# Kernel optimization log

Measured on AMD Instinct MI355X. Metric: run time of the kernel, lower is better.

Reference implementation:

```python
import jax, jax.numpy as jnp
import numpy as np

D_MODEL = 1024
N_HEADS = 16
D_K = D_MODEL // N_HEADS
D_FF = 4096
EPS = 1e-6


def setup_inputs() -> dict:
    key = jax.random.key(0)
    ks = jax.random.split(key, 8)
    s = 0.02
    return {
        "x": jax.random.normal(ks[0], (2, 2048, D_MODEL), dtype=jnp.float32),
        "Wq": jax.random.normal(ks[1], (D_MODEL, D_MODEL), dtype=jnp.float32) * s,
        "bq": jnp.zeros((D_MODEL,), jnp.float32),
        "Wk": jax.random.normal(ks[2], (D_MODEL, D_MODEL), dtype=jnp.float32) * s,
        "bk": jnp.zeros((D_MODEL,), jnp.float32),
        "Wv": jax.random.normal(ks[3], (D_MODEL, D_MODEL), dtype=jnp.float32) * s,
        "bv": jnp.zeros((D_MODEL,), jnp.float32),
        "Wo": jax.random.normal(ks[4], (D_MODEL, D_MODEL), dtype=jnp.float32) * s,
        "bo": jnp.zeros((D_MODEL,), jnp.float32),
        "W1": jax.random.normal(ks[5], (D_FF, D_MODEL), dtype=jnp.float32) * s,
        "b1": jnp.zeros((D_FF,), jnp.float32),
        "W2": jax.random.normal(ks[6], (D_MODEL, D_FF), dtype=jnp.float32) * s,
        "b2": jnp.zeros((D_MODEL,), jnp.float32),
        "g1": jnp.ones((D_MODEL,), jnp.float32),
        "be1": jnp.zeros((D_MODEL,), jnp.float32),
        "g2": jnp.ones((D_MODEL,), jnp.float32),
        "be2": jnp.zeros((D_MODEL,), jnp.float32),
    }


def _layernorm(x, gamma, beta):
    mean = x.mean(axis=-1, keepdims=True)
    var = ((x - mean) ** 2).mean(axis=-1, keepdims=True)
    return gamma * (x - mean) / jnp.sqrt(var + EPS) + beta


def _linear(x, W, b):
    # torch nn.Linear: y = x @ W.T + b
    return x @ W.T + b


def reference(x, Wq, bq, Wk, bk, Wv, bv, Wo, bo, W1, b1, W2, b2, g1, be1, g2, be2):
    B, S, _ = x.shape
    h = _layernorm(x, g1, be1)
    # project and split heads -> [B, H, S, d_k]
    Q = _linear(h, Wq, bq).reshape(B, S, N_HEADS, D_K).transpose(0, 2, 1, 3)
    K = _linear(h, Wk, bk).reshape(B, S, N_HEADS, D_K).transpose(0, 2, 1, 3)
    V = _linear(h, Wv, bv).reshape(B, S, N_HEADS, D_K).transpose(0, 2, 1, 3)
    scores = jnp.einsum("bhqd,bhkd->bhqk", Q, K) / jnp.sqrt(jnp.float32(D_K))
    attn = jax.nn.softmax(scores, axis=-1)
    ctx = jnp.einsum("bhqk,bhkd->bhqd", attn, V)
    ctx = ctx.transpose(0, 2, 1, 3).reshape(B, S, D_MODEL)
    x = x + _linear(ctx, Wo, bo)
    h2 = _layernorm(x, g2, be2)
    ff = _linear(jax.nn.gelu(_linear(h2, W1, b1), approximate=False), W2, b2)
    return x + ff
```

## Files before the change

kernel.cpp:

```cpp
#include <hip/hip_runtime.h>
#include <stdint.h>

#define D_MODEL 1024
#define N_HEADS 16
#define DKH     64
#define D_FF    4096
#define BATCH   2
#define SEQ     2048
#define M_TOK   (BATCH*SEQ)

typedef unsigned short u16;
typedef __attribute__((ext_vector_type(8))) short short8;
typedef __attribute__((ext_vector_type(4))) float f32x4;

__device__ __forceinline__ u16 f2b(float f){
  union { float f; uint32_t i; } c; c.f = f;
  uint32_t x = c.i;
  uint32_t r = x + 0x7fffu + ((x >> 16) & 1u);
  return (u16)(r >> 16);
}

__device__ __forceinline__ uint32_t pk_bf16(float a, float b){
  uint32_t d;
  asm("v_cvt_pk_bf16_f32 %0, %1, %2" : "=v"(d) : "v"(a), "v"(b));
  return d;
}

__device__ __forceinline__ void gl_lds16(const u16* g, u16* l){
  __builtin_amdgcn_global_load_lds(
      (const __attribute__((address_space(1))) void*)g,
      (__attribute__((address_space(3))) void*)l, 16, 0, 0);
}

#define MFMA16(a,b,c) __builtin_amdgcn_mfma_f32_16x16x32_bf16((a),(b),(c),0,0,0)

__global__ __launch_bounds__(256) void cvt_ln_kernel(
    const float* __restrict__ s0, const float* __restrict__ s1,
    const float* __restrict__ s2, const float* __restrict__ s3,
    const float* __restrict__ s4, const float* __restrict__ s5,
    u16* __restrict__ d0, u16* __restrict__ d1, u16* __restrict__ d2,
    u16* __restrict__ d3, u16* __restrict__ d4, u16* __restrict__ d5,
    const float* __restrict__ X, const float* __restrict__ G,
    const float* __restrict__ Bt, u16* __restrict__ O)
{
  __shared__ float psum[4], psum2[4];
  if (blockIdx.y == 6){
    const int row = blockIdx.x;
    const int t = threadIdx.x;
    float4 xv = *(const float4*)&X[(size_t)row * D_MODEL + t * 4];
    float s  = xv.x + xv.y + xv.z + xv.w;
    float s2 = xv.x*xv.x + xv.y*xv.y + xv.z*xv.z + xv.w*xv.w;
    #pragma unroll
    for (int off = 32; off >= 1; off >>= 1){
      s  += __shfl_down(s,  off, 64);
      s2 += __shfl_down(s2, off, 64);
    }
    const int wv = t >> 6, ln = t & 63;
    if (ln == 0){ psum[wv] = s; psum2[wv] = s2; }
    __syncthreads();
    float ts  = psum[0] + psum[1] + psum[2] + psum[3];
    float ts2 = psum2[0] + psum2[1] + psum2[2] + psum2[3];
    float mean = ts * (1.f / D_MODEL);
    float var  = ts2 * (1.f / D_MODEL) - mean * mean;
    float rstd = rsqrtf(var + 1e-6f);
    float4 g4 = *(const float4*)&G[t * 4];
    float4 b4 = *(const float4*)&Bt[t * 4];
    ushort4 o;
    o.x = f2b(g4.x * (xv.x - mean) * rstd + b4.x);
    o.y = f2b(g4.y * (xv.y - mean) * rstd + b4.y);
    o.z = f2b(g4.z * (xv.z - mean) * rstd + b4.z);
    o.w = f2b(g4.w * (xv.w - mean) * rstd + b4.w);
    *(ushort4*)&O[(size_t)row * D_MODEL + t * 4] = o;
    return;
  }
  const float* s; u16* d; int n;
  switch (blockIdx.y){
    case 0: s=s0; d=d0; n=D_MODEL*D_MODEL; break;
    case 1: s=s1; d=d1; n=D_MODEL*D_MODEL; break;
    case 2: s=s2; d=d2; n=D_MODEL*D_MODEL; break;
    case 3: s=s3; d=d3; n=D_MODEL*D_MODEL; break;
    case 4: s=s4; d=d4; n=D_FF*D_MODEL;   break;
    default: s=s5; d=d5; n=D_MODEL*D_FF;  break;
  }
  int i = (blockIdx.x * 256 + threadIdx.x) * 4;
  if (i < n){
    float4 f = *(const float4*)&s[i];
    ushort4 o; o.x = f2b(f.x); o.y = f2b(f.y); o.z = f2b(f.z); o.w = f2b(f.w);
    *(ushort4*)&d[i] = o;
  }
}

__global__ __launch_bounds__(256) void ln_kernel(
    const float* __restrict__ X, const float* __restrict__ G,
    const float* __restrict__ Bt, u16* __restrict__ O)
{
  const int row = blockIdx.x;
  const int t = threadIdx.x;
  float4 xv = *(const float4*)&X[(size_t)row * D_MODEL + t * 4];
  float s  = xv.x + xv.y + xv.z + xv.w;
  float s2 = xv.x*xv.x + xv.y*xv.y + xv.z*xv.z + xv.w*xv.w;
  #pragma unroll
  for (int off = 32; off >= 1; off >>= 1){
    s  += __shfl_down(s,  off, 64);
    s2 += __shfl_down(s2, off, 64);
  }
  __shared__ float psum[4], psum2[4];
  const int wv = t >> 6, ln = t & 63;
  if (ln == 0){ psum[wv] = s; psum2[wv] = s2; }
  __syncthreads();
  float ts  = psum[0] + psum[1] + psum[2] + psum[3];
  float ts2 = psum2[0] + psum2[1] + psum2[2] + psum2[3];
  float mean = ts * (1.f / D_MODEL);
  float var  = ts2 * (1.f / D_MODEL) - mean * mean;
  float rstd = rsqrtf(var + 1e-6f);
  float4 g4 = *(const float4*)&G[t * 4];
  float4 b4 = *(const float4*)&Bt[t * 4];
  ushort4 o;
  o.x = f2b(g4.x * (xv.x - mean) * rstd + b4.x);
  o.y = f2b(g4.y * (xv.y - mean) * rstd + b4.y);
  o.z = f2b(g4.z * (xv.z - mean) * rstd + b4.z);
  o.w = f2b(g4.w * (xv.w - mean) * rstd + b4.w);
  *(ushort4*)&O[(size_t)row * D_MODEL + t * 4] = o;
}

template<int EPI, int OUTF, int TM, int TN, int BK>
__global__ __launch_bounds__(256,2) void gemm_bt(
    const u16* __restrict__ A, const u16* __restrict__ W,
    const float* __restrict__ bias, const float* resid,
    void* Cout, int K, int Ndim)
{
  constexpr int MI = TM / 32;
  constexpr int NJ = TN / 32;
  constexpr int CPR = BK / 8;
  constexpr int RPI = 512 / BK;
  constexpr int nAw = TM * BK / 512 / 4;
  constexpr int nBw = TN * BK / 512 / 4;
  __shared__ __align__(16) u16 sA[TM*BK];
  __shared__ __align__(16) u16 sB[TN*BK];
  const int t = threadIdx.x;
  const int w = t >> 6, lane = t & 63, lr = lane & 15, quad = lane >> 4;
  const int wm = (w & 1) * (TM/2), wn = (w >> 1) * (TN/2);
  const int m0 = blockIdx.x * TM, n0 = blockIdx.y * TN;
  const int sub = lane / CPR;
  const int cl  = lane % CPR;

  f32x4 acc[MI][NJ];
  #pragma unroll
  for (int i = 0; i < MI; i++)
    #pragma unroll
    for (int j = 0; j < NJ; j++) acc[i][j] = (f32x4){0.f,0.f,0.f,0.f};

  for (int k0 = 0; k0 < K; k0 += BK){
    __syncthreads();
    #pragma unroll
    for (int it = 0; it < nAw; it++){
      int R = (w*nAw + it) * RPI;
      int gr = R + sub;
      int gc = (cl ^ (gr & 7)) * 8;
      gl_lds16(&A[(size_t)(m0 + gr) * K + k0 + gc], &sA[R * BK]);
    }
    #pragma unroll
    for (int it = 0; it < nBw; it++){
      int R = (w*nBw + it) * RPI;
      int gr = R + sub;
      int gc = (cl ^ (gr & 7)) * 8;
      gl_lds16(&W[(size_t)(n0 + gr) * K + k0 + gc], &sB[R * BK]);
    }
    __syncthreads();
    #pragma unroll
    for (int ks = 0; ks < BK/32; ks++){
      short8 af[MI], bfr[NJ];
      #pragma unroll
      for (int i = 0; i < MI; i++)
        af[i]  = *(const short8*)&sA[(wm + i*16 + lr)*BK + (((ks*4 + quad) ^ (lr & 7)) * 8)];
      #pragma unroll
      for (int j = 0; j < NJ; j++)
        bfr[j] = *(const short8*)&sB[(wn + j*16 + lr)*BK + (((ks*4 + quad) ^ (lr & 7)) * 8)];
      #pragma unroll
      for (int i = 0; i < MI; i++)
        #pragma unroll
        for (int j = 0; j < NJ; j++)
          acc[i][j] = MFMA16(af[i], bfr[j], acc[i][j]);
    }
  }

  #pragma unroll
  for (int j = 0; j < NJ; j++){
    int gn = n0 + wn + j*16 + lr;
    float bb = bias[gn];
    #pragma unroll
    for (int i = 0; i < MI; i++){
      #pragma unroll
      for (int r = 0; r < 4; r++){
        int gm = m0 + wm + i*16 + quad*4 + r;
        size_t idx = (size_t)gm * Ndim + gn;
        float v = acc[i][j][r] + bb;
        if (EPI == 1){
          float p = v * (1.59576912f + 0.07135481f * v * v);
          float e = __builtin_amdgcn_exp2f(-1.44269504f * p);
          v = v * __builtin_amdgcn_rcpf(1.f + e);
        }
        if (EPI == 2) v += resid[idx];
        if (OUTF) ((float*)Cout)[idx] = v;
        else      ((u16*)Cout)[idx] = f2b(v);
      }
    }
  }
}

__global__ __launch_bounds__(256,2) void gemm_qkv(
    const u16* __restrict__ A,
    const u16* __restrict__ Wq, const float* __restrict__ bq,
    const u16* __restrict__ Wk, const float* __restrict__ bk,
    const u16* __restrict__ Wv, const float* __restrict__ bv,
    u16* __restrict__ Qo, u16* __restrict__ Ko, u16* __restrict__ Vo)
{
  __shared__ __align__(16) u16 smem[2*128*64];
  u16* sA = smem;
  u16* sB = smem + 128*64;
  const u16* W; const float* bias; float scale;
  if (blockIdx.z == 0){ W = Wq; bias = bq; scale = 0.125f * 1.44269504f; }
  else if (blockIdx.z == 1){ W = Wk; bias = bk; scale = 1.f; }
  else { W = Wv; bias = bv; scale = 1.f; }

  const int t = threadIdx.x;
  const int w = t >> 6, lane = t & 63, lr = lane & 15, quad = lane >> 4;
  const int wm = (w & 1) * 64, wn = (w >> 1) * 64;
  const int m0 = blockIdx.x * 128, n0 = blockIdx.y * 128;
  const int srow = lane >> 3;
  const int scol = ((lane & 7) ^ srow) * 8;
  const int K = D_MODEL;

  f32x4 acc[4][4];
  #pragma unroll
  for (int i = 0; i < 4; i++)
    #pragma unroll
    for (int j = 0; j < 4; j++) acc[i][j] = (f32x4){0.f,0.f,0.f,0.f};

  for (int k0 = 0; k0 < K; k0 += 64){
    __syncthreads();
    #pragma unroll
    for (int it = 0; it < 4; it++){
      gl_lds16(&A[(size_t)(m0 + it*32 + w*8 + srow) * K + k0 + scol], &sA[(it*32 + w*8) * 64]);
      gl_lds16(&W[(size_t)(n0 + it*32 + w*8 + srow) * K + k0 + scol], &sB[(it*32 + w*8) * 64]);
    }
    __syncthreads();
    #pragma unroll
    for (int ks = 0; ks < 2; ks++){
      short8 af[4], bfr[4];
      #pragma unroll
      for (int i = 0; i < 4; i++)
        af[i]  = *(const short8*)&sA[(wm + i*16 + lr)*64 + (((ks*4 + quad) ^ (lr & 7)) * 8)];
      #pragma unroll
      for (int j = 0; j < 4; j++)
        bfr[j] = *(const short8*)&sB[(wn + j*16 + lr)*64 + (((ks*4 + quad) ^ (lr & 7)) * 8)];
      #pragma unroll
      for (int i = 0; i < 4; i++)
        #pragma unroll
        for (int j = 0; j < 4; j++)
          acc[i][j] = MFMA16(af[i], bfr[j], acc[i][j]);
    }
  }

  if (blockIdx.z == 2){
    __syncthreads();
    #pragma unroll
    for (int j = 0; j < 4; j++){
      int dl = wn + j*16 + lr;
      float bb = bias[n0 + dl];
      #pragma unroll
      for (int i = 0; i < 4; i++){
        #pragma unroll
        for (int r = 0; r < 4; r++){
          int tok = wm + i*16 + quad*4 + r;
          int phys = (((tok >> 3) ^ (dl & 7)) * 8) + (tok & 7);
          smem[dl*128 + phys] = f2b(acc[i][j][r] + bb);
        }
      }
    }
    __syncthreads();
    const int b = m0 >> 11, sq0 = m0 & 2047, hh0 = n0 >> 6;
    #pragma unroll
    for (int it = 0; it < 8; it++){
      int idx = it*256 + t;
      int drow = idx >> 4, c = idx & 15;
      float4 val = *(const float4*)&smem[drow*128 + ((c ^ (drow & 7)) * 8)];
      int hh = hh0 + (drow >> 6), d = drow & 63;
      *(float4*)&Vo[(((size_t)(b*N_HEADS + hh))*DKH + d)*SEQ + sq0 + c*8] = val;
    }
    return;
  }

  u16* out = (blockIdx.z == 0) ? Qo : Ko;
  #pragma unroll
  for (int j = 0; j < 4; j++){
    int gn = n0 + wn + j*16 + lr;
    int hh = gn >> 6, d = gn & 63;
    float bb = bias[gn];
    #pragma unroll
    for (int i = 0; i < 4; i++){
      #pragma unroll
      for (int r = 0; r < 4; r++){
        int gm = m0 + wm + i*16 + quad*4 + r;
        int b = gm >> 11, sq = gm & 2047;
        float v = (acc[i][j][r] + bb) * scale;
        out[(((size_t)(b * N_HEADS + hh)) * SEQ + sq) * DKH + d] = f2b(v);
      }
    }
  }
}

__global__ __launch_bounds__(512,2) void attn_kernel(
    const u16* __restrict__ Q, const u16* __restrict__ K,
    const u16* __restrict__ Vt, u16* __restrict__ ctx)
{
  __shared__ __align__(16) u16 sK[128*64];
  __shared__ __align__(16) u16 sVt[64*128];
  __shared__ __align__(16) u16 sP[8*16*128];

  const int t = threadIdx.x, w = t >> 6, lane = t & 63;
  const int lr = lane & 15, quad = lane >> 4;
  const int bh = blockIdx.x;
  const int q0 = blockIdx.y * 128;
  const u16* Qp = Q + ((size_t)bh * SEQ + q0) * DKH;
  const u16* Kp = K + (size_t)bh * SEQ * DKH;
  const u16* Vp = Vt + (size_t)bh * DKH * SEQ;

  short8 qf[2];
  #pragma unroll
  for (int ks = 0; ks < 2; ks++)
    qf[ks] = *(const short8*)&Qp[(size_t)(w*16 + lr) * DKH + ks*32 + quad*8];

  short8 ones;
  #pragma unroll
  for (int e = 0; e < 8; e++) ones[e] = (short)0x3F80;

  f32x4 acco[4];
  f32x4 accl;
  accl = (f32x4){0.f,0.f,0.f,0.f};
  #pragma unroll
  for (int jc = 0; jc < 4; jc++) acco[jc] = (f32x4){0.f,0.f,0.f,0.f};

  const int srow = lane >> 3;
  const int sc8  = ((lane & 7) ^ srow) * 8;
  const int lro  = lane >> 4, cl = lane & 15;

  for (int kt = 0; kt < SEQ/128; kt++){
    const int s0 = kt * 128;
    __syncthreads();
    #pragma unroll
    for (int it = 0; it < 2; it++)
      gl_lds16(&Kp[(size_t)(s0 + it*64 + w*8 + srow) * DKH + sc8],
               &sK[(it*64 + w*8) * 64]);
    #pragma unroll
    for (int it = 0; it < 2; it++){
      int R = w*8 + it*4;
      int gr = R + lro;
      int gc = (cl ^ (gr & 7)) * 8;
      gl_lds16(&Vp[(size_t)gr * SEQ + s0 + gc], &sVt[R * 128]);
    }
    __syncthreads();

    f32x4 st_[8];
    #pragma unroll
    for (int j = 0; j < 8; j++) st_[j] = (f32x4){0.f,0.f,0.f,0.f};
    #pragma unroll
    for (int ks = 0; ks < 2; ks++){
      #pragma unroll
      for (int j = 0; j < 8; j++){
        short8 kf = *(const short8*)&sK[(j*16 + lr)*64 + (((ks*4 + quad) ^ (lr & 7)) * 8)];
        st_[j] = MFMA16(kf, qf[ks], st_[j]);
      }
    }

    #pragma unroll
    for (int j = 0; j < 8; j++){
      float p0 = __builtin_amdgcn_exp2f(st_[j][0]);
      float p1 = __builtin_amdgcn_exp2f(st_[j][1]);
      float p2 = __builtin_amdgcn_exp2f(st_[j][2]);
      float p3 = __builtin_amdgcn_exp2f(st_[j][3]);
      uint2 pv; pv.x = pk_bf16(p0, p1); pv.y = pk_bf16(p2, p3);
      int c = j*2 + (quad >> 1);
      *(uint2*)&sP[w*2048 + lr*128 + ((c ^ (lr & 7)) * 8) + (quad & 1)*4] = pv;
    }

    #pragma unroll
    for (int ks = 0; ks < 4; ks++){
      short8 pf = *(const short8*)&sP[w*2048 + lr*128 + (((ks*4 + quad) ^ (lr & 7)) * 8)];
      accl = MFMA16(pf, ones, accl);
      #pragma unroll
      for (int jc = 0; jc < 4; jc++){
        short8 vf = *(const short8*)&sVt[(jc*16 + lr)*128 + (((ks*4 + quad) ^ (lr & 7)) * 8)];
        acco[jc] = MFMA16(pf, vf, acco[jc]);
      }
    }
  }

  const int bq = bh >> 4, hh = bh & 15;
  u16* op = ctx + ((size_t)bq * SEQ + q0) * D_MODEL + hh * DKH;
  #pragma unroll
  for (int r = 0; r < 4; r++){
    float rl = 1.f / accl[r];
    int row = w*16 + quad*4 + r;
    #pragma unroll
    for (int jc = 0; jc < 4; jc++)
      op[(size_t)row * D_MODEL + jc*16 + lr] = f2b(acco[jc][r] * rl);
  }
}

extern "C" void kernel_launch(void* const* d_in, const int* in_sizes, int n_in,
                              void* d_out, int out_size, void* d_ws, size_t ws_size,
                              hipStream_t stream)
{
  const float* x   = (const float*)d_in[0];
  const float* Wq  = (const float*)d_in[1];
  const float* bq  = (const float*)d_in[2];
  const float* Wk  = (const float*)d_in[3];
  const float* bk  = (const float*)d_in[4];
  const float* Wv  = (const float*)d_in[5];
  const float* bv  = (const float*)d_in[6];
  const float* Wo  = (const float*)d_in[7];
  const float* bo  = (const float*)d_in[8];
  const float* W1  = (const float*)d_in[9];
  const float* b1  = (const float*)d_in[10];
  const float* W2  = (const float*)d_in[11];
  const float* b2  = (const float*)d_in[12];
  const float* g1  = (const float*)d_in[13];
  const float* be1 = (const float*)d_in[14];
  const float* g2  = (const float*)d_in[15];
  const float* be2 = (const float*)d_in[16];

  char* ws = (char*)d_ws;
  const size_t MB = 1024ull * 1024ull;
  u16* wqb = (u16*)(ws + 0*MB);
  u16* wkb = (u16*)(ws + 2*MB);
  u16* wvb = (u16*)(ws + 4*MB);
  u16* wob = (u16*)(ws + 6*MB);
  u16* w1b = (u16*)(ws + 8*MB);
  u16* w2b = (u16*)(ws + 16*MB);
  u16* h   = (u16*)(ws + 24*MB);
  u16* q   = (u16*)(ws + 32*MB);
  u16* k   = (u16*)(ws + 40*MB);
  u16* ctx = (u16*)(ws + 48*MB);
  u16* vt  = (u16*)(ws + 56*MB);
  u16* ff  = (u16*)(ws + 32*MB);
  u16* h2  = h;
  float* x1 = (float*)d_out;

  cvt_ln_kernel<<<dim3(4096, 7), 256, 0, stream>>>(
      Wq, Wk, Wv, Wo, W1, W2, wqb, wkb, wvb, wob, w1b, w2b,
      x, g1, be1, h);

  gemm_qkv<<<dim3(M_TOK/128, D_MODEL/128, 3), 256, 0, stream>>>(
      h, wqb, bq, wkb, bk, wvb, bv, q, k, vt);
  attn_kernel<<<dim3(BATCH*N_HEADS, SEQ/128), 512, 0, stream>>>(q, k, vt, ctx);
  gemm_bt<2,1,64,128,128><<<dim3(M_TOK/64, D_MODEL/128), 256, 0, stream>>>(
      ctx, wob, bo, x, (void*)x1, D_MODEL, D_MODEL);
  ln_kernel<<<M_TOK, 256, 0, stream>>>(x1, g2, be2, h2);
  gemm_bt<1,0,128,128,64><<<dim3(M_TOK/128, D_FF/128), 256, 0, stream>>>(
      h2, w1b, b1, nullptr, (void*)ff, D_MODEL, D_FF);
  gemm_bt<2,1,64,128,128><<<dim3(M_TOK/64, D_MODEL/128), 256, 0, stream>>>(
      ff, w2b, b2, x1, d_out, D_FF, D_MODEL);
}
```

Before: 327.4 us.

## Give each attention wave two query tiles to reuse K/V fragments

```diff
diff --git a/kernel.cpp b/kernel.cpp
--- a/kernel.cpp
+++ b/kernel.cpp
@@ -124,7 +124,7 @@
 }
 
 template<int EPI, int OUTF, int TM, int TN, int BK>
-__global__ __launch_bounds__(256,2) void gemm_bt(
+__device__ __forceinline__ void gemm_core(
     const u16* __restrict__ A, const u16* __restrict__ W,
     const float* __restrict__ bias, const float* resid,
     void* Cout, int K, int Ndim)
@@ -208,6 +208,21 @@
   }
 }
 
+__global__ __launch_bounds__(256,2) void gemm_wo(
+    const u16* __restrict__ A, const u16* __restrict__ W,
+    const float* __restrict__ bias, const float* resid, void* Cout)
+{ gemm_core<2,1,64,128,128>(A, W, bias, resid, Cout, D_MODEL, D_MODEL); }
+
+__global__ __launch_bounds__(256,2) void gemm_ff1(
+    const u16* __restrict__ A, const u16* __restrict__ W,
+    const float* __restrict__ bias, void* Cout)
+{ gemm_core<1,0,128,128,64>(A, W, bias, nullptr, Cout, D_MODEL, D_FF); }
+
+__global__ __launch_bounds__(256,2) void gemm_ff2(
+    const u16* __restrict__ A, const u16* __restrict__ W,
+    const float* __restrict__ bias, const float* resid, void* Cout)
+{ gemm_core<2,1,64,128,128>(A, W, bias, resid, Cout, D_FF, D_MODEL); }
+
 __global__ __launch_bounds__(256,2) void gemm_qkv(
     const u16* __restrict__ A,
     const u16* __restrict__ Wq, const float* __restrict__ bq,
@@ -310,13 +325,13 @@
   }
 }
 
-__global__ __launch_bounds__(512,2) void attn_kernel(
+__global__ __launch_bounds__(256,2) void attn_kernel(
     const u16* __restrict__ Q, const u16* __restrict__ K,
     const u16* __restrict__ Vt, u16* __restrict__ ctx)
 {
   __shared__ __align__(16) u16 sK[128*64];
   __shared__ __align__(16) u16 sVt[64*128];
-  __shared__ __align__(16) u16 sP[8*16*128];
+  __shared__ __align__(16) u16 sP[4*32*128];
 
   const int t = threadIdx.x, w = t >> 6, lane = t & 63;
   const int lr = lane & 15, quad = lane >> 4;
@@ -326,72 +341,84 @@
   const u16* Kp = K + (size_t)bh * SEQ * DKH;
   const u16* Vp = Vt + (size_t)bh * DKH * SEQ;
 
-  short8 qf[2];
-  #pragma unroll
-  for (int ks = 0; ks < 2; ks++)
-    qf[ks] = *(const short8*)&Qp[(size_t)(w*16 + lr) * DKH + ks*32 + quad*8];
+  short8 qf[2][2];
+  #pragma unroll
+  for (int i = 0; i < 2; i++)
+    #pragma unroll
+    for (int ks = 0; ks < 2; ks++)
+      qf[i][ks] = *(const short8*)&Qp[(size_t)(w*32 + i*16 + lr) * DKH + ks*32 + quad*8];
 
   short8 ones;
   #pragma unroll
   for (int e = 0; e < 8; e++) ones[e] = (short)0x3F80;
 
-  f32x4 acco[4];
-  f32x4 accl;
-  accl = (f32x4){0.f,0.f,0.f,0.f};
-  #pragma unroll
-  for (int jc = 0; jc < 4; jc++) acco[jc] = (f32x4){0.f,0.f,0.f,0.f};
-
-  const int srow = lane >> 3;
-  const int sc8  = ((lane & 7) ^ srow) * 8;
-  const int lro  = lane >> 4, cl = lane & 15;
+  f32x4 acco[2][4];
+  f32x4 accl[2];
+  #pragma unroll
+  for (int i = 0; i < 2; i++){
+    accl[i] = (f32x4){0.f,0.f,0.f,0.f};
+    #pragma unroll
+    for (int jc = 0; jc < 4; jc++) acco[i][jc] = (f32x4){0.f,0.f,0.f,0.f};
+  }
 
   for (int kt = 0; kt < SEQ/128; kt++){
     const int s0 = kt * 128;
     __syncthreads();
     #pragma unroll
-    for (int it = 0; it < 2; it++)
-      gl_lds16(&Kp[(size_t)(s0 + it*64 + w*8 + srow) * DKH + sc8],
-               &sK[(it*64 + w*8) * 64]);
-    #pragma unroll
-    for (int it = 0; it < 2; it++){
-      int R = w*8 + it*4;
-      int gr = R + lro;
-      int gc = (cl ^ (gr & 7)) * 8;
+    for (int it = 0; it < 4; it++){
+      int R = (w*4 + it) * 8;
+      int gr = R + (lane >> 3);
+      int gc = ((lane & 7) ^ (gr & 7)) * 8;
+      gl_lds16(&Kp[(size_t)(s0 + gr) * DKH + gc], &sK[R * 64]);
+    }
+    #pragma unroll
+    for (int it = 0; it < 4; it++){
+      int R = (w*4 + it) * 4;
+      int gr = R + (lane >> 4);
+      int gc = ((lane & 15) ^ (gr & 7)) * 8;
       gl_lds16(&Vp[(size_t)gr * SEQ + s0 + gc], &sVt[R * 128]);
     }
     __syncthreads();
 
-    f32x4 st_[8];
-    #pragma unroll
-    for (int j = 0; j < 8; j++) st_[j] = (f32x4){0.f,0.f,0.f,0.f};
+    f32x4 st_[2][8];
+    #pragma unroll
+    for (int i = 0; i < 2; i++)
+      #pragma unroll
+      for (int j = 0; j < 8; j++) st_[i][j] = (f32x4){0.f,0.f,0.f,0.f};
     #pragma unroll
     for (int ks = 0; ks < 2; ks++){
       #pragma unroll
       for (int j = 0; j < 8; j++){
         short8 kf = *(const short8*)&sK[(j*16 + lr)*64 + (((ks*4 + quad) ^ (lr & 7)) * 8)];
-        st_[j] = MFMA16(kf, qf[ks], st_[j]);
-      }
-    }
-
-    #pragma unroll
-    for (int j = 0; j < 8; j++){
-      float p0 = __builtin_amdgcn_exp2f(st_[j][0]);
-      float p1 = __builtin_amdgcn_exp2f(st_[j][1]);
-      float p2 = __builtin_amdgcn_exp2f(st_[j][2]);
-      float p3 = __builtin_amdgcn_exp2f(st_[j][3]);
-      uint2 pv; pv.x = pk_bf16(p0, p1); pv.y = pk_bf16(p2, p3);
-      int c = j*2 + (quad >> 1);
-      *(uint2*)&sP[w*2048 + lr*128 + ((c ^ (lr & 7)) * 8) + (quad & 1)*4] = pv;
-    }
+        st_[0][j] = MFMA16(kf, qf[0][ks], st_[0][j]);
+        st_[1][j] = MFMA16(kf, qf[1][ks], st_[1][j]);
+      }
+    }
+
+    #pragma unroll
+    for (int i = 0; i < 2; i++)
+      #pragma unroll
+      for (int j = 0; j < 8; j++){
+        float p0 = __builtin_amdgcn_exp2f(st_[i][j][0]);
+        float p1 = __builtin_amdgcn_exp2f(st_[i][j][1]);
+        float p2 = __builtin_amdgcn_exp2f(st_[i][j][2]);
+        float p3 = __builtin_amdgcn_exp2f(st_[i][j][3]);
+        uint2 pv; pv.x = pk_bf16(p0, p1); pv.y = pk_bf16(p2, p3);
+        int c = j*2 + (quad >> 1);
+        *(uint2*)&sP[w*4096 + (i*16 + lr)*128 + ((c ^ (lr & 7)) * 8) + (quad & 1)*4] = pv;
+      }
 
     #pragma unroll
     for (int ks = 0; ks < 4; ks++){
-      short8 pf = *(const short8*)&sP[w*2048 + lr*128 + (((ks*4 + quad) ^ (lr & 7)) * 8)];
-      accl = MFMA16(pf, ones, accl);
+      short8 pf0 = *(const short8*)&sP[w*4096 + lr*128        + (((ks*4 + quad) ^ (lr & 7)) * 8)];
+      short8 pf1 = *(const short8*)&sP[w*4096 + (16 + lr)*128 + (((ks*4 + quad) ^ (lr & 7)) * 8)];
+      accl[0] = MFMA16(pf0, ones, accl[0]);
+      accl[1] = MFMA16(pf1, ones, accl[1]);
       #pragma unroll
       for (int jc = 0; jc < 4; jc++){
         short8 vf = *(const short8*)&sVt[(jc*16 + lr)*128 + (((ks*4 + quad) ^ (lr & 7)) * 8)];
-        acco[jc] = MFMA16(pf, vf, acco[jc]);
+        acco[0][jc] = MFMA16(pf0, vf, acco[0][jc]);
+        acco[1][jc] = MFMA16(pf1, vf, acco[1][jc]);
       }
     }
   }
@@ -399,12 +426,15 @@
   const int bq = bh >> 4, hh = bh & 15;
   u16* op = ctx + ((size_t)bq * SEQ + q0) * D_MODEL + hh * DKH;
   #pragma unroll
-  for (int r = 0; r < 4; r++){
-    float rl = 1.f / accl[r];
-    int row = w*16 + quad*4 + r;
-    #pragma unroll
-    for (int jc = 0; jc < 4; jc++)
-      op[(size_t)row * D_MODEL + jc*16 + lr] = f2b(acco[jc][r] * rl);
+  for (int i = 0; i < 2; i++){
+    #pragma unroll
+    for (int r = 0; r < 4; r++){
+      float rl = 1.f / accl[i][r];
+      int row = w*32 + i*16 + quad*4 + r;
+      #pragma unroll
+      for (int jc = 0; jc < 4; jc++)
+        op[(size_t)row * D_MODEL + jc*16 + lr] = f2b(acco[i][jc][r] * rl);
+    }
   }
 }
 
@@ -453,12 +483,12 @@
 
   gemm_qkv<<<dim3(M_TOK/128, D_MODEL/128, 3), 256, 0, stream>>>(
       h, wqb, bq, wkb, bk, wvb, bv, q, k, vt);
-  attn_kernel<<<dim3(BATCH*N_HEADS, SEQ/128), 512, 0, stream>>>(q, k, vt, ctx);
-  gemm_bt<2,1,64,128,128><<<dim3(M_TOK/64, D_MODEL/128), 256, 0, stream>>>(
-      ctx, wob, bo, x, (void*)x1, D_MODEL, D_MODEL);
+  attn_kernel<<<dim3(BATCH*N_HEADS, SEQ/128), 256, 0, stream>>>(q, k, vt, ctx);
+  gemm_wo<<<dim3(M_TOK/64, D_MODEL/128), 256, 0, stream>>>(
+      ctx, wob, bo, x, (void*)x1);
   ln_kernel<<<M_TOK, 256, 0, stream>>>(x1, g2, be2, h2);
-  gemm_bt<1,0,128,128,64><<<dim3(M_TOK/128, D_FF/128), 256, 0, stream>>>(
-      h2, w1b, b1, nullptr, (void*)ff, D_MODEL, D_FF);
-  gemm_bt<2,1,64,128,128><<<dim3(M_TOK/64, D_MODEL/128), 256, 0, stream>>>(
-      ff, w2b, b2, x1, d_out, D_FF, D_MODEL);
-}
+  gemm_ff1<<<dim3(M_TOK/128, D_FF/128), 256, 0, stream>>>(
+      h2, w1b, b1, (void*)ff);
+  gemm_ff2<<<dim3(M_TOK/64, D_MODEL/128), 256, 0, stream>>>(
+      ff, w2b, b2, x1, d_out);
+}
```

Result: no change. 330.5 us (+0.9%).
